# Kernel tuning notes

Hardware: AMD Instinct MI355X
Metric: run time of the kernel (lower is better)

## Reference

```python
import jax, jax.numpy as jnp
import numpy as np

D_MODEL = 1024
N_HEADS = 16
FEAT_DIM = 16   # q/k head dim before feature-map expansion
V_DIM = 64      # v head dim = d_model / n_heads
EPS = 1e-12


def taylor_exp(x):
    """2nd-order Taylor approx feature map of exp(q^T k / sqrt(d)).
    x: (b, h, l, d) -> (b, h, l, 1 + d + d^2)
    f(x) = [1, x / d^{1/4}, vec(x x^T) / (sqrt(2) * sqrt(d))]
    """
    d = x.shape[-1]
    rd = jnp.sqrt(jnp.float32(d))          # sqrt(d)
    rrd = jnp.sqrt(rd)                     # d^{1/4}
    r2 = jnp.sqrt(jnp.float32(2.0))
    x2 = (x[..., :, None] * x[..., None, :]).reshape(*x.shape[:-1], d * d) / r2
    ones = jnp.ones(x.shape[:-1] + (1,), dtype=x.dtype)
    return jnp.concatenate([ones, x / rrd, x2 / rd], axis=-1)


def setup_inputs() -> dict:
    key = jax.random.key(0)
    k0, k1, k2, k3, k4 = jax.random.split(key, 5)
    b, l = 2, 2048
    scale = 1.0 / np.sqrt(D_MODEL)
    return {
        "hidden_states": jax.random.normal(k0, (b, l, D_MODEL), dtype=jnp.float32),
        "Wq": jax.random.normal(k1, (D_MODEL, N_HEADS * FEAT_DIM), dtype=jnp.float32) * scale,
        "Wk": jax.random.normal(k2, (D_MODEL, N_HEADS * FEAT_DIM), dtype=jnp.float32) * scale,
        "Wv": jax.random.normal(k3, (D_MODEL, N_HEADS * V_DIM), dtype=jnp.float32) * scale,
        "Wo": jax.random.normal(k4, (N_HEADS * V_DIM, D_MODEL), dtype=jnp.float32) * scale,
    }


def reference(hidden_states, Wq, Wk, Wv, Wo):
    b, l, _ = hidden_states.shape
    # projections -> (b, h, l, d)
    q = (hidden_states @ Wq).reshape(b, l, N_HEADS, FEAT_DIM).transpose(0, 2, 1, 3)
    k = (hidden_states @ Wk).reshape(b, l, N_HEADS, FEAT_DIM).transpose(0, 2, 1, 3)
    v = (hidden_states @ Wv).reshape(b, l, N_HEADS, V_DIM).transpose(0, 2, 1, 3)

    qf = taylor_exp(q)  # (b, h, l, 273)
    kf = taylor_exp(k)

    # causal linear attention (naive parallel form used by the torch module)
    A = jnp.einsum('bhnf,bhmf->bhnm', qf, kf)
    A = jnp.tril(A)
    y = jnp.einsum('bhnm,bhme->bhne', A, v)
    # denominator: q_f . cumsum(k_f)
    z = 1.0 / (jnp.einsum('bhlf,bhlf->bhl', qf, jnp.cumsum(kf, axis=2)) + EPS)
    y = y * z[..., None]

    out = y.transpose(0, 2, 1, 3).reshape(b, l, N_HEADS * V_DIM) @ Wo
    return out
```

## Files before the change

### kernel.cpp

```cpp
#include <hip/hip_runtime.h>
#include <hip/hip_bf16.h>

#define BATCH 2
#define LSEQ 2048
#define DMODEL 1024
#define NH 16
#define DQK 16
#define DV 64
#define FDIM 273
#define CHUNK 128
#define NCH (LSEQ / CHUNK)
#define ROWS (BATCH * LSEQ)
#define NBH (BATCH * NH)
#define NBC (NBH * NCH)
#define QKVW 1536
#define C2 0.17677669529663687f

typedef short bf16x8 __attribute__((ext_vector_type(8)));
typedef float f32x4 __attribute__((ext_vector_type(4)));

__device__ __forceinline__ unsigned short f2bf(float f) {
  __hip_bfloat16 h = __float2bfloat16(f);
  unsigned short u; __builtin_memcpy(&u, &h, 2); return u;
}
__device__ __forceinline__ float bf2f(unsigned short u) {
  unsigned int v = (unsigned int)u << 16; float f; __builtin_memcpy(&f, &v, 4); return f;
}

__device__ __forceinline__ void storeC(float* C, size_t off, float v) { C[off] = v; }
__device__ __forceinline__ void storeC(unsigned short* C, size_t off, float v) {
  C[off] = f2bf(v);
}

__global__ __launch_bounds__(256) void prep(
    const float* __restrict__ hs,
    const float* __restrict__ Wq, const float* __restrict__ Wk,
    const float* __restrict__ Wv, const float* __restrict__ Wo,
    unsigned short* __restrict__ hsb,
    unsigned short* __restrict__ wqt, unsigned short* __restrict__ wkt,
    unsigned short* __restrict__ wvt, unsigned short* __restrict__ wot) {
  __shared__ float t[32][33];
  if (blockIdx.z == 4) {
    int bid = blockIdx.y * 32 + blockIdx.x;
    const float4* in4 = (const float4*)hs;
#pragma unroll
    for (int k = 0; k < 4; k++) {
      int i = bid * 1024 + k * 256 + threadIdx.x;
      float4 v = in4[i];
      ushort4 o = {f2bf(v.x), f2bf(v.y), f2bf(v.z), f2bf(v.w)};
      ((ushort4*)hsb)[i] = o;
    }
    return;
  }
  const float* W; unsigned short* Wt; int N;
  switch (blockIdx.z) {
    case 0: W = Wq; Wt = wqt; N = 256; break;
    case 1: W = Wk; Wt = wkt; N = 256; break;
    case 2: W = Wv; Wt = wvt; N = 1024; break;
    default: W = Wo; Wt = wot; N = 1024; break;
  }
  const int nb = blockIdx.x * 32;
  if (nb >= N) return;
  const int kb = blockIdx.y * 32;
  const int tx = threadIdx.x & 31, ty4 = (threadIdx.x >> 5) * 4;
#pragma unroll
  for (int r = 0; r < 4; r++)
    t[ty4 + r][tx] = W[(size_t)(kb + ty4 + r) * N + nb + tx];
  __syncthreads();
#pragma unroll
  for (int r = 0; r < 4; r++)
    Wt[(size_t)(nb + ty4 + r) * DMODEL + kb + tx] = f2bf(t[tx][ty4 + r]);
}

template <typename CT>
__global__ __launch_bounds__(256) void gemm_pipe(
    const unsigned short* __restrict__ A, const unsigned short* __restrict__ Bt,
    CT* __restrict__ C, int M, int N, int K) {
  __shared__ unsigned short Sbuf[4 * 8192];
  const int tid = threadIdx.x;
  const int nwg = gridDim.x * gridDim.y;
  const int bid0 = blockIdx.y * gridDim.x + blockIdx.x;
  const int bid = (bid0 & 7) * (nwg >> 3) + (bid0 >> 3);
  const int bm = (bid / gridDim.x) * 128, bn = (bid % gridDim.x) * 128;
  const int lane = tid & 63;
  const int w = tid >> 6;
  const int qr = (w >> 1) * 64, qc = (w & 1) * 64;
  const int nk = K >> 5;
  f32x4 acc[4][4] = {};

  const unsigned short* gbase[4];
  int loff[4];
#pragma unroll
  for (int j = 0; j < 4; ++j) {
    int c = j * 256 + tid;
    int isB = c >> 9;
    int cc = c & 511;
    int row = ((cc >> 6) << 4) + (cc & 15);
    int kh = (cc >> 4) & 3;
    gbase[j] = (isB ? Bt + (size_t)(bn + row) * K : A + (size_t)(bm + row) * K) + kh * 8;
    loff[j] = isB * 4096 + cc * 8;
  }
  auto stage = [&](int t) {
    unsigned short* Sb = Sbuf + (size_t)(t & 3) * 8192;
#pragma unroll
    for (int j = 0; j < 4; ++j)
      __builtin_amdgcn_global_load_lds(
          (const __attribute__((address_space(1))) unsigned int*)(const void*)(gbase[j] + (t << 5)),
          (__attribute__((address_space(3))) unsigned int*)(Sb + loff[j]), 16, 0, 0);
  };

  stage(0); stage(1); stage(2);

  for (int tt = 0; tt < nk; tt += 2) {
    if (tt + 3 < nk) {
      stage(tt + 3);
      asm volatile("s_waitcnt vmcnt(8)" ::: "memory");
    } else {
      asm volatile("s_waitcnt vmcnt(0)" ::: "memory");
    }
    __builtin_amdgcn_s_barrier();
    asm volatile("" ::: "memory");

    const unsigned short* Ab0 = Sbuf + (size_t)(tt & 3) * 8192;
    const unsigned short* Ab1 = Sbuf + (size_t)((tt + 1) & 3) * 8192;
    bf16x8 a0[4], b0[4], a1[4], b1[4];
#pragma unroll
    for (int i = 0; i < 4; ++i) {
      a0[i] = *(const bf16x8*)(Ab0 + ((qr >> 4) + i) * 512 + lane * 8);
      b0[i] = *(const bf16x8*)(Ab0 + 4096 + ((qc >> 4) + i) * 512 + lane * 8);
      a1[i] = *(const bf16x8*)(Ab1 + ((qr >> 4) + i) * 512 + lane * 8);
      b1[i] = *(const bf16x8*)(Ab1 + 4096 + ((qc >> 4) + i) * 512 + lane * 8);
    }
    __builtin_amdgcn_s_setprio(1);
#pragma unroll
    for (int i = 0; i < 4; ++i)
#pragma unroll
      for (int jj = 0; jj < 4; ++jj)
        acc[i][jj] = __builtin_amdgcn_mfma_f32_16x16x32_bf16(a0[i], b0[jj], acc[i][jj], 0, 0, 0);
#pragma unroll
    for (int i = 0; i < 4; ++i)
#pragma unroll
      for (int jj = 0; jj < 4; ++jj)
        acc[i][jj] = __builtin_amdgcn_mfma_f32_16x16x32_bf16(a1[i], b1[jj], acc[i][jj], 0, 0, 0);
    __builtin_amdgcn_s_setprio(0);

    asm volatile("" ::: "memory");
    __builtin_amdgcn_s_barrier();
    asm volatile("" ::: "memory");
    if (tt + 4 < nk) stage(tt + 4);
  }

  const int cn = lane & 15, r0 = (lane >> 4) * 4;
#pragma unroll
  for (int i = 0; i < 4; ++i)
#pragma unroll
    for (int jj = 0; jj < 4; ++jj) {
      size_t base = (size_t)(bm + qr + i * 16 + r0) * N + bn + qc + jj * 16 + cn;
#pragma unroll
      for (int r = 0; r < 4; ++r) storeC(C, base + (size_t)r * N, acc[i][jj][r]);
    }
}

__device__ __forceinline__ void stage_Vp(const unsigned short* __restrict__ qkvb,
                                         int row0, int h, int tid, short* Vp) {
#pragma unroll
  for (int it = 0; it < 4; it++) {
    int t = it * 256 + tid;
    int j = t >> 3, e0 = (t & 7) * 8;
    bf16x8 v8 = *(const bf16x8*)(qkvb + (size_t)(row0 + j) * QKVW + 512 + h * 64 + e0);
    int jg = j >> 3, jj = j & 7;
#pragma unroll
    for (int u = 0; u < 8; u++) {
      int e = e0 + u;
      Vp[((e >> 4) * 4 + (jg >> 2)) * 512 + ((jg & 3) * 16 + (e & 15)) * 8 + jj] =
          v8[u];
    }
  }
  {
    int n = tid & 15, jgrp = tid >> 4;
    bf16x8 v8;
#pragma unroll
    for (int u = 0; u < 8; u++) v8[u] = (n == 0) ? (short)0x3F80 : (short)0;
    *(bf16x8*)(Vp + (16 + (jgrp >> 2)) * 512 + ((jgrp & 3) * 16 + n) * 8) = v8;
  }
}

__global__ __launch_bounds__(256) void chunk_sums_mfma(
    const unsigned short* __restrict__ qkvb, unsigned short* __restrict__ Sfrag) {
  const int c = blockIdx.x, bh = blockIdx.y;
  const int b = bh >> 4, h = bh & 15;
  const int tid = threadIdx.x;
  const int lane = tid & 63, w = tid >> 6;
  const int row0 = b * LSEQ + c * CHUNK;

  __shared__ float ksT[16 * 132];
  __shared__ short SH[56 * 512];
  short* Vp = SH;
  short* Kf0 = SH + 20 * 512;
  short* Kf1 = SH + 38 * 512;

  {
    int i = tid >> 1, d0 = (tid & 1) * 8;
    bf16x8 k8 = *(const bf16x8*)(qkvb + (size_t)(row0 + i) * QKVW + 256 + h * 16 + d0);
#pragma unroll
    for (int j = 0; j < 8; j++) ksT[(d0 + j) * 132 + i] = bf2f((unsigned short)k8[j]);
  }
  stage_Vp(qkvb, row0, h, tid, Vp);
  __syncthreads();

  auto gen = [&](int kt, short* dst) {
    for (int o = tid; o < 1152; o += 256) {
      int mt = o >> 6, w6 = o & 63;
      int kh = w6 >> 4, m = w6 & 15;
      int f = mt * 16 + m;
      int i0 = kt * 32 + kh * 8;
      bf16x8 v8;
      if (f == 0) {
#pragma unroll
        for (int j = 0; j < 8; j++) v8[j] = (short)0x3F80;
      } else if (f < 17) {
        const float* ka = &ksT[(f - 1) * 132 + i0];
        float4 a0 = *(const float4*)ka, a1 = *(const float4*)(ka + 4);
        v8[0] = (short)f2bf(0.5f * a0.x); v8[1] = (short)f2bf(0.5f * a0.y);
        v8[2] = (short)f2bf(0.5f * a0.z); v8[3] = (short)f2bf(0.5f * a0.w);
        v8[4] = (short)f2bf(0.5f * a1.x); v8[5] = (short)f2bf(0.5f * a1.y);
        v8[6] = (short)f2bf(0.5f * a1.z); v8[7] = (short)f2bf(0.5f * a1.w);
      } else if (f < FDIM) {
        int ix = f - 17;
        const float* ka = &ksT[(ix >> 4) * 132 + i0];
        const float* kb2 = &ksT[(ix & 15) * 132 + i0];
        float4 a0 = *(const float4*)ka, a1 = *(const float4*)(ka + 4);
        float4 b0 = *(const float4*)kb2, b1 = *(const float4*)(kb2 + 4);
        v8[0] = (short)f2bf(C2 * a0.x * b0.x); v8[1] = (short)f2bf(C2 * a0.y * b0.y);
        v8[2] = (short)f2bf(C2 * a0.z * b0.z); v8[3] = (short)f2bf(C2 * a0.w * b0.w);
        v8[4] = (short)f2bf(C2 * a1.x * b1.x); v8[5] = (short)f2bf(C2 * a1.y * b1.y);
        v8[6] = (short)f2bf(C2 * a1.z * b1.z); v8[7] = (short)f2bf(C2 * a1.w * b1.w);
      } else {
#pragma unroll
        for (int j = 0; j < 8; j++) v8[j] = 0;
      }
      *(bf16x8*)(dst + mt * 512 + (kh * 16 + m) * 8) = v8;
    }
  };

  gen(0, Kf0);
  __syncthreads();

  f32x4 acc[5][5] = {};
  const int nmt = (w < 2) ? 5 : 4;
  for (int kt = 0; kt < 4; kt++) {
    short* cur = (kt & 1) ? Kf1 : Kf0;
    if (kt < 3) gen(kt + 1, (kt & 1) ? Kf0 : Kf1);
    bf16x8 bv[5];
#pragma unroll
    for (int nt = 0; nt < 5; nt++)
      bv[nt] = *(const bf16x8*)(Vp + (nt * 4 + kt) * 512 + lane * 8);
#pragma unroll
    for (int t2 = 0; t2 < 5; t2++) {
      if (t2 < nmt) {
        int mt = w + t2 * 4;
        bf16x8 av = *(const bf16x8*)(cur + mt * 512 + lane * 8);
#pragma unroll
        for (int nt = 0; nt < 5; nt++)
          acc[t2][nt] = __builtin_amdgcn_mfma_f32_16x16x32_bf16(av, bv[nt], acc[t2][nt], 0, 0, 0);
      }
    }
    __syncthreads();
  }

  const int cl = lane & 15, r0q = (lane >> 4) * 4;
#pragma unroll
  for (int t2 = 0; t2 < 5; t2++) {
    if (t2 < nmt) {
      int mt = w + t2 * 4;
#pragma unroll
      for (int reg = 0; reg < 4; reg++) {
        int f = mt * 16 + r0q + reg;
#pragma unroll
        for (int nt = 0; nt < 5; nt++) {
          int e = nt * 16 + cl;
          SH[((f >> 5) * 5 + nt) * 512 + (((f >> 3) & 3) * 16 + (e & 15)) * 8 + (f & 7)] =
              (short)f2bf(acc[t2][nt][reg]);
        }
      }
    }
  }
  __syncthreads();
  unsigned short* dst = Sfrag + ((size_t)bh * NCH + c) * 45 * 512;
  for (int o = tid; o < 2880; o += 256)
    *(bf16x8*)(dst + o * 8) = *(const bf16x8*)(SH + o * 8);
}

__global__ __launch_bounds__(64) void prefix_scan_frag(
    const unsigned short* __restrict__ Sfrag, unsigned short* __restrict__ PG) {
  const int kt5 = blockIdx.x, bh = blockIdx.y;
  const int lane = threadIdx.x;
  float run[8] = {0.f, 0.f, 0.f, 0.f, 0.f, 0.f, 0.f, 0.f};
  const size_t base = ((size_t)bh * NCH * 45 + kt5) * 512 + lane * 8;
#pragma unroll
  for (int cc = 0; cc < NCH; cc++) {
    size_t a = base + (size_t)cc * 45 * 512;
    bf16x8 s8 = *(const bf16x8*)(Sfrag + a);
    bf16x8 o8;
#pragma unroll
    for (int j = 0; j < 8; j++) {
      o8[j] = (short)f2bf(run[j]);
      run[j] += bf2f((unsigned short)s8[j]);
    }
    *(bf16x8*)(PG + a) = o8;
  }
}

__global__ __launch_bounds__(256, 3) void attn_mfma(
    const unsigned short* __restrict__ qkvb, const unsigned short* __restrict__ PG,
    unsigned short* __restrict__ ybuf) {
  const int c = blockIdx.x, bh = blockIdx.y;
  const int b = bh >> 4, h = bh & 15;
  const int tid = threadIdx.x;
  const int lane = tid & 63, w = tid >> 6;
  const int row0 = b * LSEQ + c * CHUNK;

  __shared__ short U[26624];
  __shared__ float denL[128];
  unsigned short* Uu = (unsigned short*)U;

  const int qrow = (w >> 1) * 64 + lane;
  const int shalf = w & 1;
  bf16x8 qa = *(const bf16x8*)(qkvb + (size_t)(row0 + qrow) * QKVW + h * 16);
  bf16x8 qb = *(const bf16x8*)(qkvb + (size_t)(row0 + qrow) * QKVW + h * 16 + 8);

  for (int t = tid; t < 1024; t += 256) {
    int isK = t >> 9;
    int tt = t & 511;
    int i = tt >> 2, kh = tt & 3;
    bf16x8 v8 = {0, 0, 0, 0, 0, 0, 0, 0};
    if (kh < 2)
      v8 = *(const bf16x8*)(qkvb + (size_t)(row0 + i) * QKVW + isK * 256 + h * 16 + kh * 8);
    *(bf16x8*)(U + isK * 4096 + (i >> 4) * 512 + (kh * 16 + (i & 15)) * 8) = v8;
  }
  __syncthreads();

  {
    bf16x8 aq[2];
#pragma unroll
    for (int mi = 0; mi < 2; mi++)
      aq[mi] = *(const bf16x8*)(U + (w * 2 + mi) * 512 + lane * 8);
    f32x4 S[2][8] = {};
#pragma unroll
    for (int nt = 0; nt < 8; nt++) {
      bf16x8 bk = *(const bf16x8*)(U + 4096 + nt * 512 + lane * 8);
#pragma unroll
      for (int mi = 0; mi < 2; mi++)
        S[mi][nt] = __builtin_amdgcn_mfma_f32_16x16x32_bf16(aq[mi], bk, S[mi][nt], 0, 0, 0);
    }
    const int cl = lane & 15, r0q = (lane >> 4) * 4;
#pragma unroll
    for (int mi = 0; mi < 2; mi++)
#pragma unroll
      for (int nt = 0; nt < 8; nt++)
#pragma unroll
        for (int reg = 0; reg < 4; reg++) {
          int i = (w * 2 + mi) * 16 + r0q + reg;
          int j = nt * 16 + cl;
          float s = S[mi][nt][reg];
          float aij = (j <= i) ? fmaf(s, fmaf(s, 0.03125f, 0.25f), 1.0f) : 0.0f;
          U[10240 + ((i >> 4) * 4 + (j >> 5)) * 512 +
            (((j >> 3) & 3) * 16 + (i & 15)) * 8 + (j & 7)] = (short)f2bf(aij);
        }
  }
  __syncthreads();
  stage_Vp(qkvb, row0, h, tid, U);
  __syncthreads();

  f32x4 Y[2][5] = {};
#pragma unroll
  for (int kc = 0; kc < 4; kc++) {
    bf16x8 a2[2];
#pragma unroll
    for (int mi = 0; mi < 2; mi++)
      a2[mi] = *(const bf16x8*)(U + 10240 + ((w * 2 + mi) * 4 + kc) * 512 + lane * 8);
#pragma unroll
    for (int nt = 0; nt < 5; nt++) {
      bf16x8 b2 = *(const bf16x8*)(U + (nt * 4 + kc) * 512 + lane * 8);
#pragma unroll
      for (int mi = 0; mi < 2; mi++)
        Y[mi][nt] = __builtin_amdgcn_mfma_f32_16x16x32_bf16(a2[mi], b2, Y[mi][nt], 0, 0, 0);
    }
  }
  __syncthreads();

  unsigned short* qbase = Uu + (qrow >> 4) * 512 + (qrow & 15) * 8;
  const unsigned short* pgl = PG + ((size_t)bh * NCH + c) * 45 * 512 + lane * 8;

#define GEN_VK(vk, ftl, qv, cq)                                         \
  {                                                                     \
    bf16x8 v8;                                                          \
    _Pragma("unroll")                                                   \
    for (int j = 0; j < 8; j++) {                                       \
      int f = (vk) * 8 + j;                                             \
      float qf;                                                         \
      if (f == 0) qf = 1.0f;                                            \
      else if (f < 17) qf = 0.5f * qv[f - 1];                           \
      else if (f < FDIM) { int ix = f - 17; qf = cq[ix >> 4] * qv[ix & 15]; } \
      else qf = 0.0f;                                                   \
      v8[j] = (short)f2bf(qf);                                          \
    }                                                                   \
    *(bf16x8*)(qbase + (ftl) * 4096 + ((vk) & 3) * 128) = v8;           \
  }

  {
    float qv[16], cq[16];
#pragma unroll
    for (int j = 0; j < 8; j++) {
      qv[j] = bf2f((unsigned short)qa[j]);
      qv[8 + j] = bf2f((unsigned short)qb[j]);
    }
#pragma unroll
    for (int j = 0; j < 16; j++) cq[j] = C2 * qv[j];
    if (shalf == 0) {
#pragma unroll
      for (int vk = 0; vk < 10; vk++) GEN_VK(vk, vk >> 2, qv, cq);
    } else {
#pragma unroll
      for (int vk = 10; vk < 20; vk++) GEN_VK(vk, vk >> 2, qv, cq);
    }
  }
  __syncthreads();

#pragma unroll
  for (int ft = 0; ft < 5; ft++) {
    bf16x8 b3[5];
#pragma unroll
    for (int nt = 0; nt < 5; nt++)
      b3[nt] = *(const bf16x8*)(pgl + (ft * 5 + nt) * 512);
    bf16x8 a3[2];
#pragma unroll
    for (int mi = 0; mi < 2; mi++)
      a3[mi] = *(const bf16x8*)(U + ft * 4096 + (w * 2 + mi) * 512 + lane * 8);
#pragma unroll
    for (int nt = 0; nt < 5; nt++)
#pragma unroll
      for (int mi = 0; mi < 2; mi++)
        Y[mi][nt] = __builtin_amdgcn_mfma_f32_16x16x32_bf16(a3[mi], b3[nt], Y[mi][nt], 0, 0, 0);
  }
  __syncthreads();

  {
    float qv[16], cq[16];
#pragma unroll
    for (int j = 0; j < 8; j++) {
      qv[j] = bf2f((unsigned short)qa[j]);
      qv[8 + j] = bf2f((unsigned short)qb[j]);
    }
#pragma unroll
    for (int j = 0; j < 16; j++) cq[j] = C2 * qv[j];
    if (shalf == 0) {
#pragma unroll
      for (int vk = 20; vk < 28; vk++) GEN_VK(vk, (vk >> 2) - 5, qv, cq);
    } else {
#pragma unroll
      for (int vk = 28; vk < 36; vk++) GEN_VK(vk, (vk >> 2) - 5, qv, cq);
    }
  }
  __syncthreads();

#pragma unroll
  for (int ft = 5; ft < 9; ft++) {
    bf16x8 b3[5];
#pragma unroll
    for (int nt = 0; nt < 5; nt++)
      b3[nt] = *(const bf16x8*)(pgl + (ft * 5 + nt) * 512);
    bf16x8 a3[2];
#pragma unroll
    for (int mi = 0; mi < 2; mi++)
      a3[mi] = *(const bf16x8*)(U + (ft - 5) * 4096 + (w * 2 + mi) * 512 + lane * 8);
#pragma unroll
    for (int nt = 0; nt < 5; nt++)
#pragma unroll
      for (int mi = 0; mi < 2; mi++)
        Y[mi][nt] = __builtin_amdgcn_mfma_f32_16x16x32_bf16(a3[mi], b3[nt], Y[mi][nt], 0, 0, 0);
  }
#undef GEN_VK

  const int cl = lane & 15, r0q = (lane >> 4) * 4;
  if (cl == 0) {
#pragma unroll
    for (int mi = 0; mi < 2; mi++)
#pragma unroll
      for (int reg = 0; reg < 4; reg++)
        denL[(w * 2 + mi) * 16 + r0q + reg] = Y[mi][4][reg];
  }
  __syncthreads();
#pragma unroll
  for (int mi = 0; mi < 2; mi++) {
    float invd[4];
#pragma unroll
    for (int reg = 0; reg < 4; reg++)
      invd[reg] = 1.0f / (denL[(w * 2 + mi) * 16 + r0q + reg] + 1e-12f);
#pragma unroll
    for (int nt = 0; nt < 4; nt++)
#pragma unroll
      for (int reg = 0; reg < 4; reg++) {
        int i = (w * 2 + mi) * 16 + r0q + reg;
        int e = nt * 16 + cl;
        ybuf[(size_t)(row0 + i) * (NH * DV) + h * DV + e] =
            f2bf(Y[mi][nt][reg] * invd[reg]);
      }
  }
}

extern "C" void kernel_launch(void* const* d_in, const int* in_sizes, int n_in,
                              void* d_out, int out_size, void* d_ws, size_t ws_size,
                              hipStream_t stream) {
  const float* hs = (const float*)d_in[0];
  const float* Wq = (const float*)d_in[1];
  const float* Wk = (const float*)d_in[2];
  const float* Wv = (const float*)d_in[3];
  const float* Wo = (const float*)d_in[4];
  float* out = (float*)d_out;

  unsigned short* qkvb  = (unsigned short*)d_ws;
  unsigned short* Sfrag = qkvb + (size_t)ROWS * QKVW;
  unsigned short* PG    = Sfrag + (size_t)NBC * 45 * 512;
  unsigned short* hsb   = PG + (size_t)NBC * 45 * 512;
  unsigned short* yb    = hsb;
  unsigned short* wqt   = hsb + (size_t)ROWS * DMODEL;
  unsigned short* wkt   = wqt + (size_t)(NH * DQK) * DMODEL;
  unsigned short* wvt   = wkt + (size_t)(NH * DQK) * DMODEL;
  unsigned short* wot   = wvt + (size_t)(NH * DV) * DMODEL;

  prep<<<dim3(32, 32, 5), 256, 0, stream>>>(hs, Wq, Wk, Wv, Wo, hsb, wqt, wkt, wvt, wot);

  gemm_pipe<unsigned short><<<dim3(QKVW / 128, ROWS / 128), 256, 0, stream>>>(
      hsb, wqt, qkvb, ROWS, QKVW, DMODEL);

  chunk_sums_mfma<<<dim3(NCH, NBH), 256, 0, stream>>>(qkvb, Sfrag);
  prefix_scan_frag<<<dim3(45, NBH), 64, 0, stream>>>(Sfrag, PG);
  attn_mfma<<<dim3(NCH, NBH), 256, 0, stream>>>(qkvb, PG, yb);

  gemm_pipe<float><<<dim3(DMODEL / 128, ROWS / 128), 256, 0, stream>>>(
      yb, wot, out, ROWS, DMODEL, DMODEL);
}
```

Measured before the change: 168.0 us.

## Fuse chunk sums, prefix scan and attention into one kernel with grid barriers

Merges the three attention-stage kernels into a single persistent launch of 512 blocks. Two software grid barriers (atomic counters reset in the prep kernel) separate the chunk-sum, prefix-scan and attention phases, and shared memory is unioned across phases. The prefix scan is spread over the waves of the fused grid. This removes two kernel launches and their gaps, but it depends on all 512 blocks being co-resident (launch bounds 256,2) to avoid deadlock, and the barrier spin adds its own cost.

```diff
diff --git a/kernel.cpp b/kernel.cpp
--- a/kernel.cpp
+++ b/kernel.cpp
@@ -32,15 +32,31 @@
   C[off] = f2bf(v);
 }
 
+__device__ __forceinline__ void grid_bar(unsigned int* cnt, int tid) {
+  __syncthreads();
+  if (tid == 0) {
+    __threadfence();
+    __hip_atomic_fetch_add(cnt, 1u, __ATOMIC_RELAXED, __HIP_MEMORY_SCOPE_AGENT);
+    while (__hip_atomic_load(cnt, __ATOMIC_RELAXED, __HIP_MEMORY_SCOPE_AGENT) < NBC)
+      __builtin_amdgcn_s_sleep(2);
+    __threadfence();
+  }
+  __syncthreads();
+}
+
 __global__ __launch_bounds__(256) void prep(
     const float* __restrict__ hs,
     const float* __restrict__ Wq, const float* __restrict__ Wk,
     const float* __restrict__ Wv, const float* __restrict__ Wo,
     unsigned short* __restrict__ hsb,
     unsigned short* __restrict__ wqt, unsigned short* __restrict__ wkt,
-    unsigned short* __restrict__ wvt, unsigned short* __restrict__ wot) {
+    unsigned short* __restrict__ wvt, unsigned short* __restrict__ wot,
+    unsigned int* __restrict__ bar) {
   __shared__ float t[32][33];
   if (blockIdx.z == 4) {
+    if (blockIdx.x == 0 && blockIdx.y == 0 && threadIdx.x == 0) {
+      bar[0] = 0; bar[1] = 0;
+    }
     int bid = blockIdx.y * 32 + blockIdx.x;
     const float4* in4 = (const float4*)hs;
 #pragma unroll
@@ -185,327 +201,333 @@
   }
 }
 
-__global__ __launch_bounds__(256) void chunk_sums_mfma(
-    const unsigned short* __restrict__ qkvb, unsigned short* __restrict__ Sfrag) {
+__global__ __launch_bounds__(256, 2) void attn_chain(
+    const unsigned short* __restrict__ qkvb, unsigned short* __restrict__ Sfrag,
+    unsigned short* __restrict__ PG, unsigned short* __restrict__ ybuf,
+    unsigned int* __restrict__ bar) {
   const int c = blockIdx.x, bh = blockIdx.y;
   const int b = bh >> 4, h = bh & 15;
   const int tid = threadIdx.x;
   const int lane = tid & 63, w = tid >> 6;
   const int row0 = b * LSEQ + c * CHUNK;
 
-  __shared__ float ksT[16 * 132];
-  __shared__ short SH[56 * 512];
-  short* Vp = SH;
-  short* Kf0 = SH + 20 * 512;
-  short* Kf1 = SH + 38 * 512;
+  __shared__ union {
+    struct { float ksT[16 * 132]; short SH[56 * 512]; } cs;
+    struct { short U[26624]; float denL[128]; } at;
+  } S;
 
   {
-    int i = tid >> 1, d0 = (tid & 1) * 8;
-    bf16x8 k8 = *(const bf16x8*)(qkvb + (size_t)(row0 + i) * QKVW + 256 + h * 16 + d0);
-#pragma unroll
-    for (int j = 0; j < 8; j++) ksT[(d0 + j) * 132 + i] = bf2f((unsigned short)k8[j]);
-  }
-  stage_Vp(qkvb, row0, h, tid, Vp);
-  __syncthreads();
-
-  auto gen = [&](int kt, short* dst) {
-    for (int o = tid; o < 1152; o += 256) {
-      int mt = o >> 6, w6 = o & 63;
-      int kh = w6 >> 4, m = w6 & 15;
-      int f = mt * 16 + m;
-      int i0 = kt * 32 + kh * 8;
-      bf16x8 v8;
-      if (f == 0) {
-#pragma unroll
-        for (int j = 0; j < 8; j++) v8[j] = (short)0x3F80;
-      } else if (f < 17) {
-        const float* ka = &ksT[(f - 1) * 132 + i0];
-        float4 a0 = *(const float4*)ka, a1 = *(const float4*)(ka + 4);
-        v8[0] = (short)f2bf(0.5f * a0.x); v8[1] = (short)f2bf(0.5f * a0.y);
-        v8[2] = (short)f2bf(0.5f * a0.z); v8[3] = (short)f2bf(0.5f * a0.w);
-        v8[4] = (short)f2bf(0.5f * a1.x); v8[5] = (short)f2bf(0.5f * a1.y);
-        v8[6] = (short)f2bf(0.5f * a1.z); v8[7] = (short)f2bf(0.5f * a1.w);
-      } else if (f < FDIM) {
-        int ix = f - 17;
-        const float* ka = &ksT[(ix >> 4) * 132 + i0];
-        const float* kb2 = &ksT[(ix & 15) * 132 + i0];
-        float4 a0 = *(const float4*)ka, a1 = *(const float4*)(ka + 4);
-        float4 b0 = *(const float4*)kb2, b1 = *(const float4*)(kb2 + 4);
-        v8[0] = (short)f2bf(C2 * a0.x * b0.x); v8[1] = (short)f2bf(C2 * a0.y * b0.y);
-        v8[2] = (short)f2bf(C2 * a0.z * b0.z); v8[3] = (short)f2bf(C2 * a0.w * b0.w);
-        v8[4] = (short)f2bf(C2 * a1.x * b1.x); v8[5] = (short)f2bf(C2 * a1.y * b1.y);
-        v8[6] = (short)f2bf(C2 * a1.z * b1.z); v8[7] = (short)f2bf(C2 * a1.w * b1.w);
-      } else {
-#pragma unroll
-        for (int j = 0; j < 8; j++) v8[j] = 0;
-      }
-      *(bf16x8*)(dst + mt * 512 + (kh * 16 + m) * 8) = v8;
-    }
-  };
-
-  gen(0, Kf0);
-  __syncthreads();
-
-  f32x4 acc[5][5] = {};
-  const int nmt = (w < 2) ? 5 : 4;
-  for (int kt = 0; kt < 4; kt++) {
-    short* cur = (kt & 1) ? Kf1 : Kf0;
-    if (kt < 3) gen(kt + 1, (kt & 1) ? Kf0 : Kf1);
-    bf16x8 bv[5];
-#pragma unroll
-    for (int nt = 0; nt < 5; nt++)
-      bv[nt] = *(const bf16x8*)(Vp + (nt * 4 + kt) * 512 + lane * 8);
+    float* ksT = S.cs.ksT;
+    short* SH = S.cs.SH;
+    short* Vp = SH;
+    short* Kf0 = SH + 20 * 512;
+    short* Kf1 = SH + 38 * 512;
+
+    {
+      int i = tid >> 1, d0 = (tid & 1) * 8;
+      bf16x8 k8 = *(const bf16x8*)(qkvb + (size_t)(row0 + i) * QKVW + 256 + h * 16 + d0);
+#pragma unroll
+      for (int j = 0; j < 8; j++) ksT[(d0 + j) * 132 + i] = bf2f((unsigned short)k8[j]);
+    }
+    stage_Vp(qkvb, row0, h, tid, Vp);
+    __syncthreads();
+
+    auto gen = [&](int kt, short* dst) {
+      for (int o = tid; o < 1152; o += 256) {
+        int mt = o >> 6, w6 = o & 63;
+        int kh = w6 >> 4, m = w6 & 15;
+        int f = mt * 16 + m;
+        int i0 = kt * 32 + kh * 8;
+        bf16x8 v8;
+        if (f == 0) {
+#pragma unroll
+          for (int j = 0; j < 8; j++) v8[j] = (short)0x3F80;
+        } else if (f < 17) {
+          const float* ka = &ksT[(f - 1) * 132 + i0];
+          float4 a0 = *(const float4*)ka, a1 = *(const float4*)(ka + 4);
+          v8[0] = (short)f2bf(0.5f * a0.x); v8[1] = (short)f2bf(0.5f * a0.y);
+          v8[2] = (short)f2bf(0.5f * a0.z); v8[3] = (short)f2bf(0.5f * a0.w);
+          v8[4] = (short)f2bf(0.5f * a1.x); v8[5] = (short)f2bf(0.5f * a1.y);
+          v8[6] = (short)f2bf(0.5f * a1.z); v8[7] = (short)f2bf(0.5f * a1.w);
+        } else if (f < FDIM) {
+          int ix = f - 17;
+          const float* ka = &ksT[(ix >> 4) * 132 + i0];
+          const float* kb2 = &ksT[(ix & 15) * 132 + i0];
+          float4 a0 = *(const float4*)ka, a1 = *(const float4*)(ka + 4);
+          float4 b0 = *(const float4*)kb2, b1 = *(const float4*)(kb2 + 4);
+          v8[0] = (short)f2bf(C2 * a0.x * b0.x); v8[1] = (short)f2bf(C2 * a0.y * b0.y);
+          v8[2] = (short)f2bf(C2 * a0.z * b0.z); v8[3] = (short)f2bf(C2 * a0.w * b0.w);
+          v8[4] = (short)f2bf(C2 * a1.x * b1.x); v8[5] = (short)f2bf(C2 * a1.y * b1.y);
+          v8[6] = (short)f2bf(C2 * a1.z * b1.z); v8[7] = (short)f2bf(C2 * a1.w * b1.w);
+        } else {
+#pragma unroll
+          for (int j = 0; j < 8; j++) v8[j] = 0;
+        }
+        *(bf16x8*)(dst + mt * 512 + (kh * 16 + m) * 8) = v8;
+      }
+    };
+
+    gen(0, Kf0);
+    __syncthreads();
+
+    f32x4 acc[5][5] = {};
+    const int nmt = (w < 2) ? 5 : 4;
+    for (int kt = 0; kt < 4; kt++) {
+      short* cur = (kt & 1) ? Kf1 : Kf0;
+      if (kt < 3) gen(kt + 1, (kt & 1) ? Kf0 : Kf1);
+      bf16x8 bv[5];
+#pragma unroll
+      for (int nt = 0; nt < 5; nt++)
+        bv[nt] = *(const bf16x8*)(Vp + (nt * 4 + kt) * 512 + lane * 8);
+#pragma unroll
+      for (int t2 = 0; t2 < 5; t2++) {
+        if (t2 < nmt) {
+          int mt = w + t2 * 4;
+          bf16x8 av = *(const bf16x8*)(cur + mt * 512 + lane * 8);
+#pragma unroll
+          for (int nt = 0; nt < 5; nt++)
+            acc[t2][nt] = __builtin_amdgcn_mfma_f32_16x16x32_bf16(av, bv[nt], acc[t2][nt], 0, 0, 0);
+        }
+      }
+      __syncthreads();
+    }
+
+    const int cl = lane & 15, r0q = (lane >> 4) * 4;
 #pragma unroll
     for (int t2 = 0; t2 < 5; t2++) {
       if (t2 < nmt) {
         int mt = w + t2 * 4;
-        bf16x8 av = *(const bf16x8*)(cur + mt * 512 + lane * 8);
-#pragma unroll
-        for (int nt = 0; nt < 5; nt++)
-          acc[t2][nt] = __builtin_amdgcn_mfma_f32_16x16x32_bf16(av, bv[nt], acc[t2][nt], 0, 0, 0);
-      }
-    }
-    __syncthreads();
-  }
-
-  const int cl = lane & 15, r0q = (lane >> 4) * 4;
-#pragma unroll
-  for (int t2 = 0; t2 < 5; t2++) {
-    if (t2 < nmt) {
-      int mt = w + t2 * 4;
-#pragma unroll
-      for (int reg = 0; reg < 4; reg++) {
-        int f = mt * 16 + r0q + reg;
-#pragma unroll
-        for (int nt = 0; nt < 5; nt++) {
-          int e = nt * 16 + cl;
-          SH[((f >> 5) * 5 + nt) * 512 + (((f >> 3) & 3) * 16 + (e & 15)) * 8 + (f & 7)] =
-              (short)f2bf(acc[t2][nt][reg]);
+#pragma unroll
+        for (int reg = 0; reg < 4; reg++) {
+          int f = mt * 16 + r0q + reg;
+#pragma unroll
+          for (int nt = 0; nt < 5; nt++) {
+            int e = nt * 16 + cl;
+            SH[((f >> 5) * 5 + nt) * 512 + (((f >> 3) & 3) * 16 + (e & 15)) * 8 + (f & 7)] =
+                (short)f2bf(acc[t2][nt][reg]);
+          }
         }
       }
     }
-  }
-  __syncthreads();
-  unsigned short* dst = Sfrag + ((size_t)bh * NCH + c) * 45 * 512;
-  for (int o = tid; o < 2880; o += 256)
-    *(bf16x8*)(dst + o * 8) = *(const bf16x8*)(SH + o * 8);
-}
-
-__global__ __launch_bounds__(64) void prefix_scan_frag(
-    const unsigned short* __restrict__ Sfrag, unsigned short* __restrict__ PG) {
-  const int kt5 = blockIdx.x, bh = blockIdx.y;
-  const int lane = threadIdx.x;
-  float run[8] = {0.f, 0.f, 0.f, 0.f, 0.f, 0.f, 0.f, 0.f};
-  const size_t base = ((size_t)bh * NCH * 45 + kt5) * 512 + lane * 8;
-#pragma unroll
-  for (int cc = 0; cc < NCH; cc++) {
-    size_t a = base + (size_t)cc * 45 * 512;
-    bf16x8 s8 = *(const bf16x8*)(Sfrag + a);
-    bf16x8 o8;
-#pragma unroll
-    for (int j = 0; j < 8; j++) {
-      o8[j] = (short)f2bf(run[j]);
-      run[j] += bf2f((unsigned short)s8[j]);
-    }
-    *(bf16x8*)(PG + a) = o8;
-  }
-}
-
-__global__ __launch_bounds__(256, 3) void attn_mfma(
-    const unsigned short* __restrict__ qkvb, const unsigned short* __restrict__ PG,
-    unsigned short* __restrict__ ybuf) {
-  const int c = blockIdx.x, bh = blockIdx.y;
-  const int b = bh >> 4, h = bh & 15;
-  const int tid = threadIdx.x;
-  const int lane = tid & 63, w = tid >> 6;
-  const int row0 = b * LSEQ + c * CHUNK;
-
-  __shared__ short U[26624];
-  __shared__ float denL[128];
-  unsigned short* Uu = (unsigned short*)U;
-
-  const int qrow = (w >> 1) * 64 + lane;
-  const int shalf = w & 1;
-  bf16x8 qa = *(const bf16x8*)(qkvb + (size_t)(row0 + qrow) * QKVW + h * 16);
-  bf16x8 qb = *(const bf16x8*)(qkvb + (size_t)(row0 + qrow) * QKVW + h * 16 + 8);
-
-  for (int t = tid; t < 1024; t += 256) {
-    int isK = t >> 9;
-    int tt = t & 511;
-    int i = tt >> 2, kh = tt & 3;
-    bf16x8 v8 = {0, 0, 0, 0, 0, 0, 0, 0};
-    if (kh < 2)
-      v8 = *(const bf16x8*)(qkvb + (size_t)(row0 + i) * QKVW + isK * 256 + h * 16 + kh * 8);
-    *(bf16x8*)(U + isK * 4096 + (i >> 4) * 512 + (kh * 16 + (i & 15)) * 8) = v8;
-  }
-  __syncthreads();
+    __syncthreads();
+    unsigned short* dst = Sfrag + ((size_t)bh * NCH + c) * 45 * 512;
+    for (int o = tid; o < 2880; o += 256)
+      *(bf16x8*)(dst + o * 8) = *(const bf16x8*)(SH + o * 8);
+  }
+
+  grid_bar(&bar[0], tid);
 
   {
-    bf16x8 aq[2];
-#pragma unroll
-    for (int mi = 0; mi < 2; mi++)
-      aq[mi] = *(const bf16x8*)(U + (w * 2 + mi) * 512 + lane * 8);
-    f32x4 S[2][8] = {};
-#pragma unroll
-    for (int nt = 0; nt < 8; nt++) {
-      bf16x8 bk = *(const bf16x8*)(U + 4096 + nt * 512 + lane * 8);
+    int task = (blockIdx.y * gridDim.x + blockIdx.x) * 4 + w;
+    if (task < 45 * NBH) {
+      int bh2 = task / 45, kt5 = task % 45;
+      float run[8] = {0.f, 0.f, 0.f, 0.f, 0.f, 0.f, 0.f, 0.f};
+      const size_t base = ((size_t)bh2 * NCH * 45 + kt5) * 512 + lane * 8;
+#pragma unroll
+      for (int cc = 0; cc < NCH; cc++) {
+        size_t a = base + (size_t)cc * 45 * 512;
+        bf16x8 s8 = *(const bf16x8*)(Sfrag + a);
+        bf16x8 o8;
+#pragma unroll
+        for (int j = 0; j < 8; j++) {
+          o8[j] = (short)f2bf(run[j]);
+          run[j] += bf2f((unsigned short)s8[j]);
+        }
+        *(bf16x8*)(PG + a) = o8;
+      }
+    }
+  }
+
+  grid_bar(&bar[1], tid);
+
+  {
+    short* U = S.at.U;
+    float* denL = S.at.denL;
+    unsigned short* Uu = (unsigned short*)U;
+
+    const int qrow = (w >> 1) * 64 + lane;
+    const int shalf = w & 1;
+    bf16x8 qa = *(const bf16x8*)(qkvb + (size_t)(row0 + qrow) * QKVW + h * 16);
+    bf16x8 qb = *(const bf16x8*)(qkvb + (size_t)(row0 + qrow) * QKVW + h * 16 + 8);
+
+    for (int t = tid; t < 1024; t += 256) {
+      int isK = t >> 9;
+      int tt = t & 511;
+      int i = tt >> 2, kh = tt & 3;
+      bf16x8 v8 = {0, 0, 0, 0, 0, 0, 0, 0};
+      if (kh < 2)
+        v8 = *(const bf16x8*)(qkvb + (size_t)(row0 + i) * QKVW + isK * 256 + h * 16 + kh * 8);
+      *(bf16x8*)(U + isK * 4096 + (i >> 4) * 512 + (kh * 16 + (i & 15)) * 8) = v8;
+    }
+    __syncthreads();
+
+    {
+      bf16x8 aq[2];
 #pragma unroll
       for (int mi = 0; mi < 2; mi++)
-        S[mi][nt] = __builtin_amdgcn_mfma_f32_16x16x32_bf16(aq[mi], bk, S[mi][nt], 0, 0, 0);
-    }
+        aq[mi] = *(const bf16x8*)(U + (w * 2 + mi) * 512 + lane * 8);
+      f32x4 Sc[2][8] = {};
+#pragma unroll
+      for (int nt = 0; nt < 8; nt++) {
+        bf16x8 bk = *(const bf16x8*)(U + 4096 + nt * 512 + lane * 8);
+#pragma unroll
+        for (int mi = 0; mi < 2; mi++)
+          Sc[mi][nt] = __builtin_amdgcn_mfma_f32_16x16x32_bf16(aq[mi], bk, Sc[mi][nt], 0, 0, 0);
+      }
+      const int cl = lane & 15, r0q = (lane >> 4) * 4;
+#pragma unroll
+      for (int mi = 0; mi < 2; mi++)
+#pragma unroll
+        for (int nt = 0; nt < 8; nt++)
+#pragma unroll
+          for (int reg = 0; reg < 4; reg++) {
+            int i = (w * 2 + mi) * 16 + r0q + reg;
+            int j = nt * 16 + cl;
+            float s = Sc[mi][nt][reg];
+            float aij = (j <= i) ? fmaf(s, fmaf(s, 0.03125f, 0.25f), 1.0f) : 0.0f;
+            U[10240 + ((i >> 4) * 4 + (j >> 5)) * 512 +
+              (((j >> 3) & 3) * 16 + (i & 15)) * 8 + (j & 7)] = (short)f2bf(aij);
+          }
+    }
+    __syncthreads();
+    stage_Vp(qkvb, row0, h, tid, U);
+    __syncthreads();
+
+    f32x4 Y[2][5] = {};
+#pragma unroll
+    for (int kc = 0; kc < 4; kc++) {
+      bf16x8 a2[2];
+#pragma unroll
+      for (int mi = 0; mi < 2; mi++)
+        a2[mi] = *(const bf16x8*)(U + 10240 + ((w * 2 + mi) * 4 + kc) * 512 + lane * 8);
+#pragma unroll
+      for (int nt = 0; nt < 5; nt++) {
+        bf16x8 b2 = *(const bf16x8*)(U + (nt * 4 + kc) * 512 + lane * 8);
+#pragma unroll
+        for (int mi = 0; mi < 2; mi++)
+          Y[mi][nt] = __builtin_amdgcn_mfma_f32_16x16x32_bf16(a2[mi], b2, Y[mi][nt], 0, 0, 0);
+      }
+    }
+    __syncthreads();
+
+    unsigned short* qbase = Uu + (qrow >> 4) * 512 + (qrow & 15) * 8;
+    const unsigned short* pgl = PG + ((size_t)bh * NCH + c) * 45 * 512 + lane * 8;
+
+#define GEN_VK(vk, ftl, qv, cq)                                         \
+    {                                                                   \
+      bf16x8 v8;                                                        \
+      _Pragma("unroll")                                                 \
+      for (int j = 0; j < 8; j++) {                                     \
+        int f = (vk) * 8 + j;                                           \
+        float qf;                                                       \
+        if (f == 0) qf = 1.0f;                                          \
+        else if (f < 17) qf = 0.5f * qv[f - 1];                         \
+        else if (f < FDIM) { int ix = f - 17; qf = cq[ix >> 4] * qv[ix & 15]; } \
+        else qf = 0.0f;                                                 \
+        v8[j] = (short)f2bf(qf);                                        \
+      }                                                                 \
+      *(bf16x8*)(qbase + (ftl) * 4096 + ((vk) & 3) * 128) = v8;         \
+    }
+
+    {
+      float qv[16], cq[16];
+#pragma unroll
+      for (int j = 0; j < 8; j++) {
+        qv[j] = bf2f((unsigned short)qa[j]);
+        qv[8 + j] = bf2f((unsigned short)qb[j]);
+      }
+#pragma unroll
+      for (int j = 0; j < 16; j++) cq[j] = C2 * qv[j];
+      if (shalf == 0) {
+#pragma unroll
+        for (int vk = 0; vk < 10; vk++) GEN_VK(vk, vk >> 2, qv, cq);
+      } else {
+#pragma unroll
+        for (int vk = 10; vk < 20; vk++) GEN_VK(vk, vk >> 2, qv, cq);
+      }
+    }
+    __syncthreads();
+
+#pragma unroll
+    for (int ft = 0; ft < 5; ft++) {
+      bf16x8 b3[5];
+#pragma unroll
+      for (int nt = 0; nt < 5; nt++)
+        b3[nt] = *(const bf16x8*)(pgl + (ft * 5 + nt) * 512);
+      bf16x8 a3[2];
+#pragma unroll
+      for (int mi = 0; mi < 2; mi++)
+        a3[mi] = *(const bf16x8*)(U + ft * 4096 + (w * 2 + mi) * 512 + lane * 8);
+#pragma unroll
+      for (int nt = 0; nt < 5; nt++)
+#pragma unroll
+        for (int mi = 0; mi < 2; mi++)
+          Y[mi][nt] = __builtin_amdgcn_mfma_f32_16x16x32_bf16(a3[mi], b3[nt], Y[mi][nt], 0, 0, 0);
+    }
+    __syncthreads();
+
+    {
+      float qv[16], cq[16];
+#pragma unroll
+      for (int j = 0; j < 8; j++) {
+        qv[j] = bf2f((unsigned short)qa[j]);
+        qv[8 + j] = bf2f((unsigned short)qb[j]);
+      }
+#pragma unroll
+      for (int j = 0; j < 16; j++) cq[j] = C2 * qv[j];
+      if (shalf == 0) {
+#pragma unroll
+        for (int vk = 20; vk < 28; vk++) GEN_VK(vk, (vk >> 2) - 5, qv, cq);
+      } else {
+#pragma unroll
+        for (int vk = 28; vk < 36; vk++) GEN_VK(vk, (vk >> 2) - 5, qv, cq);
+      }
+    }
+    __syncthreads();
+
+#pragma unroll
+    for (int ft = 5; ft < 9; ft++) {
+      bf16x8 b3[5];
+#pragma unroll
+      for (int nt = 0; nt < 5; nt++)
+        b3[nt] = *(const bf16x8*)(pgl + (ft * 5 + nt) * 512);
+      bf16x8 a3[2];
+#pragma unroll
+      for (int mi = 0; mi < 2; mi++)
+        a3[mi] = *(const bf16x8*)(U + (ft - 5) * 4096 + (w * 2 + mi) * 512 + lane * 8);
+#pragma unroll
+      for (int nt = 0; nt < 5; nt++)
+#pragma unroll
+        for (int mi = 0; mi < 2; mi++)
+          Y[mi][nt] = __builtin_amdgcn_mfma_f32_16x16x32_bf16(a3[mi], b3[nt], Y[mi][nt], 0, 0, 0);
+    }
+#undef GEN_VK
+
     const int cl = lane & 15, r0q = (lane >> 4) * 4;
-#pragma unroll
-    for (int mi = 0; mi < 2; mi++)
-#pragma unroll
-      for (int nt = 0; nt < 8; nt++)
+    if (cl == 0) {
+#pragma unroll
+      for (int mi = 0; mi < 2; mi++)
+#pragma unroll
+        for (int reg = 0; reg < 4; reg++)
+          denL[(w * 2 + mi) * 16 + r0q + reg] = Y[mi][4][reg];
+    }
+    __syncthreads();
+#pragma unroll
+    for (int mi = 0; mi < 2; mi++) {
+      float invd[4];
+#pragma unroll
+      for (int reg = 0; reg < 4; reg++)
+        invd[reg] = 1.0f / (denL[(w * 2 + mi) * 16 + r0q + reg] + 1e-12f);
+#pragma unroll
+      for (int nt = 0; nt < 4; nt++)
 #pragma unroll
         for (int reg = 0; reg < 4; reg++) {
           int i = (w * 2 + mi) * 16 + r0q + reg;
-          int j = nt * 16 + cl;
-          float s = S[mi][nt][reg];
-          float aij = (j <= i) ? fmaf(s, fmaf(s, 0.03125f, 0.25f), 1.0f) : 0.0f;
-          U[10240 + ((i >> 4) * 4 + (j >> 5)) * 512 +
-            (((j >> 3) & 3) * 16 + (i & 15)) * 8 + (j & 7)] = (short)f2bf(aij);
+          int e = nt * 16 + cl;
+          ybuf[(size_t)(row0 + i) * (NH * DV) + h * DV + e] =
+              f2bf(Y[mi][nt][reg] * invd[reg]);
         }
-  }
-  __syncthreads();
-  stage_Vp(qkvb, row0, h, tid, U);
-  __syncthreads();
-
-  f32x4 Y[2][5] = {};
-#pragma unroll
-  for (int kc = 0; kc < 4; kc++) {
-    bf16x8 a2[2];
-#pragma unroll
-    for (int mi = 0; mi < 2; mi++)
-      a2[mi] = *(const bf16x8*)(U + 10240 + ((w * 2 + mi) * 4 + kc) * 512 + lane * 8);
-#pragma unroll
-    for (int nt = 0; nt < 5; nt++) {
-      bf16x8 b2 = *(const bf16x8*)(U + (nt * 4 + kc) * 512 + lane * 8);
-#pragma unroll
-      for (int mi = 0; mi < 2; mi++)
-        Y[mi][nt] = __builtin_amdgcn_mfma_f32_16x16x32_bf16(a2[mi], b2, Y[mi][nt], 0, 0, 0);
-    }
-  }
-  __syncthreads();
-
-  unsigned short* qbase = Uu + (qrow >> 4) * 512 + (qrow & 15) * 8;
-  const unsigned short* pgl = PG + ((size_t)bh * NCH + c) * 45 * 512 + lane * 8;
-
-#define GEN_VK(vk, ftl, qv, cq)                                         \
-  {                                                                     \
-    bf16x8 v8;                                                          \
-    _Pragma("unroll")                                                   \
-    for (int j = 0; j < 8; j++) {                                       \
-      int f = (vk) * 8 + j;                                             \
-      float qf;                                                         \
-      if (f == 0) qf = 1.0f;                                            \
-      else if (f < 17) qf = 0.5f * qv[f - 1];                           \
-      else if (f < FDIM) { int ix = f - 17; qf = cq[ix >> 4] * qv[ix & 15]; } \
-      else qf = 0.0f;                                                   \
-      v8[j] = (short)f2bf(qf);                                          \
-    }                                                                   \
-    *(bf16x8*)(qbase + (ftl) * 4096 + ((vk) & 3) * 128) = v8;           \
-  }
-
-  {
-    float qv[16], cq[16];
-#pragma unroll
-    for (int j = 0; j < 8; j++) {
-      qv[j] = bf2f((unsigned short)qa[j]);
-      qv[8 + j] = bf2f((unsigned short)qb[j]);
-    }
-#pragma unroll
-    for (int j = 0; j < 16; j++) cq[j] = C2 * qv[j];
-    if (shalf == 0) {
-#pragma unroll
-      for (int vk = 0; vk < 10; vk++) GEN_VK(vk, vk >> 2, qv, cq);
-    } else {
-#pragma unroll
-      for (int vk = 10; vk < 20; vk++) GEN_VK(vk, vk >> 2, qv, cq);
-    }
-  }
-  __syncthreads();
-
-#pragma unroll
-  for (int ft = 0; ft < 5; ft++) {
-    bf16x8 b3[5];
-#pragma unroll
-    for (int nt = 0; nt < 5; nt++)
-      b3[nt] = *(const bf16x8*)(pgl + (ft * 5 + nt) * 512);
-    bf16x8 a3[2];
-#pragma unroll
-    for (int mi = 0; mi < 2; mi++)
-      a3[mi] = *(const bf16x8*)(U + ft * 4096 + (w * 2 + mi) * 512 + lane * 8);
-#pragma unroll
-    for (int nt = 0; nt < 5; nt++)
-#pragma unroll
-      for (int mi = 0; mi < 2; mi++)
-        Y[mi][nt] = __builtin_amdgcn_mfma_f32_16x16x32_bf16(a3[mi], b3[nt], Y[mi][nt], 0, 0, 0);
-  }
-  __syncthreads();
-
-  {
-    float qv[16], cq[16];
-#pragma unroll
-    for (int j = 0; j < 8; j++) {
-      qv[j] = bf2f((unsigned short)qa[j]);
-      qv[8 + j] = bf2f((unsigned short)qb[j]);
-    }
-#pragma unroll
-    for (int j = 0; j < 16; j++) cq[j] = C2 * qv[j];
-    if (shalf == 0) {
-#pragma unroll
-      for (int vk = 20; vk < 28; vk++) GEN_VK(vk, (vk >> 2) - 5, qv, cq);
-    } else {
-#pragma unroll
-      for (int vk = 28; vk < 36; vk++) GEN_VK(vk, (vk >> 2) - 5, qv, cq);
-    }
-  }
-  __syncthreads();
-
-#pragma unroll
-  for (int ft = 5; ft < 9; ft++) {
-    bf16x8 b3[5];
-#pragma unroll
-    for (int nt = 0; nt < 5; nt++)
-      b3[nt] = *(const bf16x8*)(pgl + (ft * 5 + nt) * 512);
-    bf16x8 a3[2];
-#pragma unroll
-    for (int mi = 0; mi < 2; mi++)
-      a3[mi] = *(const bf16x8*)(U + (ft - 5) * 4096 + (w * 2 + mi) * 512 + lane * 8);
-#pragma unroll
-    for (int nt = 0; nt < 5; nt++)
-#pragma unroll
-      for (int mi = 0; mi < 2; mi++)
-        Y[mi][nt] = __builtin_amdgcn_mfma_f32_16x16x32_bf16(a3[mi], b3[nt], Y[mi][nt], 0, 0, 0);
-  }
-#undef GEN_VK
-
-  const int cl = lane & 15, r0q = (lane >> 4) * 4;
-  if (cl == 0) {
-#pragma unroll
-    for (int mi = 0; mi < 2; mi++)
-#pragma unroll
-      for (int reg = 0; reg < 4; reg++)
-        denL[(w * 2 + mi) * 16 + r0q + reg] = Y[mi][4][reg];
-  }
-  __syncthreads();
-#pragma unroll
-  for (int mi = 0; mi < 2; mi++) {
-    float invd[4];
-#pragma unroll
-    for (int reg = 0; reg < 4; reg++)
-      invd[reg] = 1.0f / (denL[(w * 2 + mi) * 16 + r0q + reg] + 1e-12f);
-#pragma unroll
-    for (int nt = 0; nt < 4; nt++)
-#pragma unroll
-      for (int reg = 0; reg < 4; reg++) {
-        int i = (w * 2 + mi) * 16 + r0q + reg;
-        int e = nt * 16 + cl;
-        ybuf[(size_t)(row0 + i) * (NH * DV) + h * DV + e] =
-            f2bf(Y[mi][nt][reg] * invd[reg]);
-      }
+    }
   }
 }
 
@@ -528,15 +550,15 @@
   unsigned short* wkt   = wqt + (size_t)(NH * DQK) * DMODEL;
   unsigned short* wvt   = wkt + (size_t)(NH * DQK) * DMODEL;
   unsigned short* wot   = wvt + (size_t)(NH * DV) * DMODEL;
-
-  prep<<<dim3(32, 32, 5), 256, 0, stream>>>(hs, Wq, Wk, Wv, Wo, hsb, wqt, wkt, wvt, wot);
+  unsigned int*   bar   = (unsigned int*)(wot + (size_t)DMODEL * DMODEL);
+
+  prep<<<dim3(32, 32, 5), 256, 0, stream>>>(hs, Wq, Wk, Wv, Wo, hsb, wqt, wkt,
+                                            wvt, wot, bar);
 
   gemm_pipe<unsigned short><<<dim3(QKVW / 128, ROWS / 128), 256, 0, stream>>>(
       hsb, wqt, qkvb, ROWS, QKVW, DMODEL);
 
-  chunk_sums_mfma<<<dim3(NCH, NBH), 256, 0, stream>>>(qkvb, Sfrag);
-  prefix_scan_frag<<<dim3(45, NBH), 64, 0, stream>>>(Sfrag, PG);
-  attn_mfma<<<dim3(NCH, NBH), 256, 0, stream>>>(qkvb, PG, yb);
+  attn_chain<<<dim3(NCH, NBH), 256, 0, stream>>>(qkvb, Sfrag, PG, yb, bar);
 
   gemm_pipe<float><<<dim3(DMODEL / 128, ROWS / 128), 256, 0, stream>>>(
       yb, wot, out, ROWS, DMODEL, DMODEL);
```

Result: slower. 289.4 us (+72.2%).
